# Performance work log

Measured on AMD Instinct MI355X. Metric: run time of the kernel, lower is better.

Reference implementation:

```python
import jax, jax.numpy as jnp
import numpy as np

N, D, R, E = 20000, 256, 12, 200000  # nodes, feat dim, relation labels, edges


def setup_inputs() -> dict:
    key = jax.random.key(0)
    ks = jax.random.split(key, 8)
    x = jax.random.normal(ks[0], (N, D), dtype=jnp.float32)
    dep_idx = jax.random.randint(ks[1], (E,), 0, N)
    rel_idx = jax.random.randint(ks[2], (E,), 0, R)
    gov_idx = jax.random.randint(ks[3], (E,), 0, N)
    # nn.Linear params: W is [out,in], y = x @ W.T + b
    W_self = jax.random.normal(ks[4], (D, D), dtype=jnp.float32) * 0.02
    b_self = jnp.zeros((D,), dtype=jnp.float32)
    # 2R relation weights: [0..R) forward labels, [R..2R) reversed '_r' labels
    W_rel = jax.random.normal(ks[5], (2 * R, D, D), dtype=jnp.float32) * 0.02
    b_rel = jax.random.normal(ks[6], (2 * R, D), dtype=jnp.float32) * 0.02
    return {"x": x, "dep_idx": dep_idx, "rel_idx": rel_idx, "gov_idx": gov_idx,
            "W_self": W_self, "b_self": b_self, "W_rel": W_rel, "b_rel": b_rel}


def reference(x, dep_idx, rel_idx, gov_idx, W_self, b_self, W_rel, b_rel):
    R_ = W_rel.shape[0] // 2
    # self transform for every node
    out = x @ W_self.T + b_self  # [N, D]
    # all-relation transform, grouped GEMM instead of per-edge Linear calls
    T = jnp.einsum('nd,rod->nro', x, W_rel)  # [N, 2R, D]
    # forward edges: dependent += W[rel] @ x[governor] + b[rel]
    msg_f = T[gov_idx, rel_idx] + b_rel[rel_idx]          # [E, D]
    # reverse edges: governor += W[rel_r] @ x[dependent] + b[rel_r]
    msg_r = T[dep_idx, rel_idx + R_] + b_rel[rel_idx + R_]  # [E, D]
    out = out.at[dep_idx].add(msg_f).at[gov_idx].add(msg_r)
    return jax.nn.relu(out)
```

## Files before the change

kernel.cpp:

```cpp
#include <hip/hip_runtime.h>
#include <cstdint>
#include <cstddef>

#define DD 256
#define NSLOT 25
#define SELFSLOT 12

typedef unsigned short u16;
typedef __bf16 bf16t;
typedef bf16t bf16x8 __attribute__((ext_vector_type(8)));
typedef unsigned short us8 __attribute__((ext_vector_type(8)));
typedef unsigned short us4 __attribute__((ext_vector_type(4)));
typedef float f32x4 __attribute__((ext_vector_type(4)));

__device__ __forceinline__ u16 f2bf(float f) {
    uint32_t u = __builtin_bit_cast(uint32_t, f);
    u += 0x7FFFu + ((u >> 16) & 1u);
    return (u16)(u >> 16);
}
__device__ __forceinline__ float bf2f(u16 h) {
    uint32_t u = ((uint32_t)h) << 16;
    return __builtin_bit_cast(float, u);
}

__global__ void k_prep(const float* __restrict__ x, const float* __restrict__ W_rel,
                       const float* __restrict__ W_self, const float* __restrict__ b_self,
                       const float* __restrict__ b_rel,
                       u16* __restrict__ xb, u16* __restrict__ Wb, float* __restrict__ ba,
                       const int* __restrict__ dep, const int* __restrict__ rel,
                       const int* __restrict__ gov, int E, int N, int SG,
                       int* __restrict__ flag, int* __restrict__ bcnt, int NDD) {
    if (blockIdx.x < 1024) {
        const int s0 = NDD;
        const int s1 = s0 + 12 * 65536;
        const int s2 = s1 + 65536;
        const int s3 = s2 + 12 * 65536;
        const int s4 = s3 + NSLOT * DD;
        int i = blockIdx.x * 256 + threadIdx.x;
        int st = 1024 * 256;
        for (; i < s4; i += st) {
            if (i < s0) {
                xb[i] = f2bf(x[i]);
            } else if (i < s1) {
                int k = i - s0; Wb[k] = f2bf(W_rel[k]);
            } else if (i < s2) {
                int k = i - s1; Wb[12 * 65536 + k] = f2bf(W_self[k]);
            } else if (i < s3) {
                int k = i - s2; Wb[13 * 65536 + k] = f2bf(W_rel[12 * 65536 + k]);
            } else {
                int k = i - s3;
                float v;
                if (k < 12 * DD) v = b_rel[k];
                else if (k < 13 * DD) v = b_self[k - 12 * DD];
                else v = b_rel[k - DD];
                ba[k] = v;
            }
        }
    } else {
        int i = (blockIdx.x - 1024) * 256 + threadIdx.x;
        int st = 512 * 256;
        for (int j = i; j < E; j += st) {
            int r = rel[j], d = dep[j], g = gov[j];
            flag[r * N + g] = 1;
            flag[(13 + r) * N + d] = 1;
            atomicAdd(&bcnt[(r / SG) * N + d], 1);
            atomicAdd(&bcnt[((13 + r) / SG) * N + g], 1);
        }
        for (int j = i; j < N; j += st) flag[SELFSLOT * N + j] = 1;
    }
}

__global__ void k_scan1d(const int* __restrict__ A, int* __restrict__ outA,
                         int* __restrict__ bsumA, int lenA, int nbA,
                         const int* __restrict__ B, int* __restrict__ outB,
                         int* __restrict__ bsumB, int lenB) {
    __shared__ int sm[256];
    const int* in; int* outp; int* bs; int len; int lb;
    if ((int)blockIdx.x < nbA) { in = A; outp = outA; bs = bsumA; len = lenA; lb = blockIdx.x; }
    else { in = B; outp = outB; bs = bsumB; len = lenB; lb = blockIdx.x - nbA; }
    int tid = threadIdx.x;
    int i = lb * 256 + tid;
    int v = (i < len) ? in[i] : 0;
    sm[tid] = v;
    __syncthreads();
    for (int off = 1; off < 256; off <<= 1) {
        int t = (tid >= off) ? sm[tid - off] : 0;
        __syncthreads();
        sm[tid] += t;
        __syncthreads();
    }
    if (i < len) outp[i] = sm[tid] - v;
    if (tid == 255) bs[lb] = sm[255];
}

__global__ void k_scan2d(const int* __restrict__ bsumA, int* __restrict__ bbasA, int nbA,
                         const int* __restrict__ bsumB, int* __restrict__ bbasB, int nbB) {
    __shared__ int sm[256];
    int t = threadIdx.x;
    for (int which = 0; which < 2; ++which) {
        const int* bsum = which ? bsumB : bsumA;
        int* bbase = which ? bbasB : bbasA;
        int nb = which ? nbB : nbA;
        int pre[8];
        int tot = 0;
        for (int j = 0; j < 8; ++j) {
            int idx = t * 8 + j;
            int v = (idx < nb) ? bsum[idx] : 0;
            pre[j] = tot;
            tot += v;
        }
        sm[t] = tot;
        __syncthreads();
        for (int off = 1; off < 256; off <<= 1) {
            int x = (t >= off) ? sm[t - off] : 0;
            __syncthreads();
            sm[t] += x;
            __syncthreads();
        }
        int base = sm[t] - tot;
        for (int j = 0; j < 8; ++j) {
            int idx = t * 8 + j;
            if (idx < nb) bbase[idx] = base + pre[j];
        }
        __syncthreads();
    }
}

__global__ void k_scan3d(int* __restrict__ pos, const int* __restrict__ bbasA,
                         const int* __restrict__ flag, int NN, int N,
                         int* __restrict__ rksrc,
                         int* __restrict__ bcsr, int* __restrict__ bcur,
                         const int* __restrict__ bbasB, int B2, int E2) {
    int i = blockIdx.x * 256 + threadIdx.x;
    if (i < NN) {
        int v = pos[i] + bbasA[i >> 8];
        pos[i] = v;
        if (i == NN - 1) pos[NN] = v + flag[i];
        if (flag[i]) {
            int slot = i / N;
            rksrc[v] = i - slot * N;
        }
    }
    if (i < B2) {
        int v = bcsr[i] + bbasB[i >> 8];
        bcsr[i] = v;
        bcur[i] = v;
    }
    if (i == 0) bcsr[B2] = E2;
}

__global__ void k_scatter(const int* __restrict__ dep, const int* __restrict__ rel,
                          const int* __restrict__ gov, int E, int N, int SG,
                          const int* __restrict__ pos,
                          int* __restrict__ cursor, int* __restrict__ epay) {
    int i = blockIdx.x * blockDim.x + threadIdx.x;
    int st = gridDim.x * blockDim.x;
    for (; i < E; i += st) {
        int r = rel[i], d = dep[i], g = gov[i];
        int g0 = r / SG;
        int p = atomicAdd(&cursor[g0 * N + d], 1);
        epay[p] = pos[r * N + g] - pos[g0 * SG * N];
        int gs = 13 + r;
        int g1 = gs / SG;
        int q = atomicAdd(&cursor[g1 * N + g], 1);
        epay[q] = pos[gs * N + d] - pos[g1 * SG * N];
    }
}

__global__ __launch_bounds__(256, 4) void k_T(
    const u16* __restrict__ xb, const u16* __restrict__ Wb, const float* __restrict__ ba,
    const int* __restrict__ pos, const int* __restrict__ rksrc, u16* __restrict__ T,
    int N, int gslot0, int Sg) {
    __shared__ u16 sm[2 * 128 * 72];
    __shared__ int s_src[128];
    u16 (*As)[72] = (u16(*)[72])sm;
    u16 (*Bs)[72] = (u16(*)[72])(sm + 128 * 72);

    const int bx = blockIdx.x;
    const int mtile = bx / (2 * Sg);
    const int rem = bx - mtile * 2 * Sg;
    const int slot = rem >> 1;
    const int n0 = (rem & 1) * 128;
    const int gslot = gslot0 + slot;
    const int u0 = pos[gslot * N];
    const int used = pos[(gslot + 1) * N] - u0;
    const int row0 = mtile * 128;
    if (row0 >= used) return;
    const int gbase = pos[gslot0 * N];
    const int tid = threadIdx.x;

    if (tid < 128) {
        int r = row0 + tid;
        s_src[tid] = rksrc[u0 + ((r < used) ? r : (used - 1))];
    }
    __syncthreads();

    const int lane = tid & 63, wv = tid >> 6;
    const int wr = wv & 1, wc = wv >> 1;
    const int l15 = lane & 15, quad = lane >> 4;
    const int srow = tid >> 1, sh = (tid & 1) * 32;
    const u16* bgp = Wb + ((size_t)gslot << 16) + (size_t)(n0 + srow) * DD + sh;

    f32x4 acc[4][4] = {};
    for (int kb = 0; kb < DD; kb += 64) {
        {
            const us8* ga = (const us8*)(xb + (size_t)s_src[srow] * DD + kb + sh);
            us8 a0 = ga[0], a1 = ga[1], a2 = ga[2], a3 = ga[3];
            *(us8*)&As[srow][sh]      = a0;
            *(us8*)&As[srow][sh + 8]  = a1;
            *(us8*)&As[srow][sh + 16] = a2;
            *(us8*)&As[srow][sh + 24] = a3;
            const us8* gb = (const us8*)(bgp + kb);
            us8 b0 = gb[0], b1 = gb[1], b2 = gb[2], b3 = gb[3];
            *(us8*)&Bs[srow][sh]      = b0;
            *(us8*)&Bs[srow][sh + 8]  = b1;
            *(us8*)&Bs[srow][sh + 16] = b2;
            *(us8*)&Bs[srow][sh + 24] = b3;
        }
        __syncthreads();
        #pragma unroll
        for (int ks = 0; ks < 2; ++ks) {
            const int kk = ks * 32 + quad * 8;
            bf16x8 af[4], bfv[4];
            #pragma unroll
            for (int mt = 0; mt < 4; ++mt)
                af[mt] = __builtin_bit_cast(bf16x8, *(const us8*)&As[wr * 64 + mt * 16 + l15][kk]);
            #pragma unroll
            for (int nt = 0; nt < 4; ++nt)
                bfv[nt] = __builtin_bit_cast(bf16x8, *(const us8*)&Bs[wc * 64 + nt * 16 + l15][kk]);
            #pragma unroll
            for (int nt = 0; nt < 4; ++nt)
                #pragma unroll
                for (int mt = 0; mt < 4; ++mt)
                    acc[nt][mt] = __builtin_amdgcn_mfma_f32_16x16x32_bf16(
                        bfv[nt], af[mt], acc[nt][mt], 0, 0, 0);
        }
        __syncthreads();
    }

    f32x4 bb[4];
    #pragma unroll
    for (int nt = 0; nt < 4; ++nt)
        bb[nt] = *(const f32x4*)(ba + gslot * DD + n0 + wc * 64 + nt * 16 + quad * 4);
    u16* trb = sm + wv * (64 * 72);
    #pragma unroll
    for (int mt = 0; mt < 4; ++mt)
        #pragma unroll
        for (int nt = 0; nt < 4; ++nt) {
            us4 t4;
            #pragma unroll
            for (int j = 0; j < 4; ++j) t4[j] = f2bf(acc[nt][mt][j] + bb[nt][j]);
            *(us4*)&trb[(size_t)(mt * 16 + l15) * 72 + nt * 16 + quad * 4] = t4;
        }
    __syncthreads();
    const int trow0 = u0 - gbase + row0 + wr * 64;
    const int half = lane & 1;
    #pragma unroll
    for (int it = 0; it < 2; ++it) {
        int r = it * 32 + (lane >> 1);
        if (row0 + wr * 64 + r < used) {
            const us8* sp = (const us8*)(trb + r * 72 + half * 32);
            us8 v0 = sp[0], v1 = sp[1], v2 = sp[2], v3 = sp[3];
            us8* dp = (us8*)(T + (size_t)(trow0 + r) * DD + n0 + wc * 64 + half * 32);
            dp[0] = v0; dp[1] = v1; dp[2] = v2; dp[3] = v3;
        }
    }
}

__global__ __launch_bounds__(256) void k_gather(
    const u16* __restrict__ T, const int* __restrict__ epay,
    const int* __restrict__ csr, const int* __restrict__ pos,
    float* __restrict__ out, int N, int bktBase, int selfKeyBase, int gfN,
    int first, int last) {
    int wid = (blockIdx.x * 256 + threadIdx.x) >> 6;
    if (wid >= N) return;
    int feat = (threadIdx.x & 63) * 4;
    f32x4 a = {0.0f, 0.0f, 0.0f, 0.0f};
    if (!first) a = *(const f32x4*)(out + (size_t)wid * DD + feat);
    if (selfKeyBase >= 0) {
        int p = pos[selfKeyBase + wid] - pos[gfN];
        us4 v = *(const us4*)(T + (size_t)p * DD + feat);
        a[0] += bf2f(v[0]); a[1] += bf2f(v[1]); a[2] += bf2f(v[2]); a[3] += bf2f(v[3]);
    }
    int beg = csr[bktBase + wid], end = csr[bktBase + wid + 1];
    f32x4 b = {0, 0, 0, 0}, c = {0, 0, 0, 0}, d4 = {0, 0, 0, 0};
    int j = beg;
    for (; j + 3 < end; j += 4) {
        int p0 = epay[j], p1 = epay[j + 1], p2 = epay[j + 2], p3 = epay[j + 3];
        us4 v0 = *(const us4*)(T + (size_t)p0 * DD + feat);
        us4 v1 = *(const us4*)(T + (size_t)p1 * DD + feat);
        us4 v2 = *(const us4*)(T + (size_t)p2 * DD + feat);
        us4 v3 = *(const us4*)(T + (size_t)p3 * DD + feat);
        a[0] += bf2f(v0[0]); a[1] += bf2f(v0[1]); a[2] += bf2f(v0[2]); a[3] += bf2f(v0[3]);
        b[0] += bf2f(v1[0]); b[1] += bf2f(v1[1]); b[2] += bf2f(v1[2]); b[3] += bf2f(v1[3]);
        c[0] += bf2f(v2[0]); c[1] += bf2f(v2[1]); c[2] += bf2f(v2[2]); c[3] += bf2f(v2[3]);
        d4[0] += bf2f(v3[0]); d4[1] += bf2f(v3[1]); d4[2] += bf2f(v3[2]); d4[3] += bf2f(v3[3]);
    }
    for (; j < end; ++j) {
        int p0 = epay[j];
        us4 v0 = *(const us4*)(T + (size_t)p0 * DD + feat);
        a[0] += bf2f(v0[0]); a[1] += bf2f(v0[1]); a[2] += bf2f(v0[2]); a[3] += bf2f(v0[3]);
    }
    a[0] += b[0] + c[0] + d4[0];
    a[1] += b[1] + c[1] + d4[1];
    a[2] += b[2] + c[2] + d4[2];
    a[3] += b[3] + c[3] + d4[3];
    if (last) {
        a[0] = fmaxf(a[0], 0.0f); a[1] = fmaxf(a[1], 0.0f);
        a[2] = fmaxf(a[2], 0.0f); a[3] = fmaxf(a[3], 0.0f);
    }
    *(f32x4*)(out + (size_t)wid * DD + feat) = a;
}

extern "C" void kernel_launch(void* const* d_in, const int* in_sizes, int n_in,
                              void* d_out, int out_size, void* d_ws, size_t ws_size,
                              hipStream_t stream) {
    const float* x      = (const float*)d_in[0];
    const int*   dep    = (const int*)  d_in[1];
    const int*   rel    = (const int*)  d_in[2];
    const int*   gov    = (const int*)  d_in[3];
    const float* W_self = (const float*)d_in[4];
    const float* b_self = (const float*)d_in[5];
    const float* W_rel  = (const float*)d_in[6];
    const float* b_rel  = (const float*)d_in[7];
    float* out = (float*)d_out;

    const int N  = in_sizes[0] / DD;
    const int E  = in_sizes[1];
    const int NN = NSLOT * N;

    char* w = (char*)d_ws;
    auto alloc = [&](size_t bytes) {
        char* p = w;
        w += (bytes + 255) & ~(size_t)255;
        return p;
    };
    u16* xb    = (u16*)alloc((size_t)N * DD * sizeof(u16));
    u16* Wb    = (u16*)alloc((size_t)NSLOT * DD * DD * sizeof(u16));
    float* ba  = (float*)alloc((size_t)NSLOT * DD * sizeof(float));
    int* flag  = (int*)alloc((size_t)NN * sizeof(int));
    int* pos   = (int*)alloc(((size_t)NN + 1) * sizeof(int));
    int* rksrc = (int*)alloc(((size_t)2 * E + N) * sizeof(int));
    int* bcnt  = (int*)alloc((size_t)6 * N * sizeof(int));
    int* bcsr  = (int*)alloc(((size_t)6 * N + 1) * sizeof(int));
    int* bcur  = (int*)alloc((size_t)6 * N * sizeof(int));
    int* bsumA = (int*)alloc((size_t)2048 * sizeof(int));
    int* bbasA = (int*)alloc((size_t)2048 * sizeof(int));
    int* bsumB = (int*)alloc((size_t)2048 * sizeof(int));
    int* bbasB = (int*)alloc((size_t)2048 * sizeof(int));
    int* epay  = (int*)alloc((size_t)2 * E * sizeof(int));

    size_t used = (size_t)(w - (char*)d_ws);
    size_t avail = (ws_size > used) ? (ws_size - used) : 0;

    int NGROUP = 2, SG = 13;
    for (int ng = 1; ng <= 5; ++ng) {
        int sg = (NSLOT + ng - 1) / ng;
        size_t maxB = 0;
        for (int g = 0; g < ng; ++g) {
            int s0 = g * sg, s1 = s0 + sg; if (s1 > NSLOT) s1 = NSLOT;
            if (s0 >= NSLOT) break;
            int hasSelf = (s0 <= SELFSLOT && SELFSLOT < s1) ? 1 : 0;
            size_t rels = (size_t)(s1 - s0 - hasSelf);
            size_t rows = rels * N; if (rows > (size_t)2 * E) rows = (size_t)2 * E;
            rows += hasSelf ? (size_t)N : 0;
            if (rows > maxB) maxB = rows;
        }
        if (maxB * ((size_t)DD * 2) <= avail) { NGROUP = ng; SG = sg; break; }
        NGROUP = ng + 1; SG = (NSLOT + NGROUP - 1) / NGROUP;
    }
    u16* T = (u16*)w;
    const int B2 = NGROUP * N;

    hipMemsetAsync(flag, 0, (size_t)NN * sizeof(int), stream);
    hipMemsetAsync(bcnt, 0, (size_t)B2 * sizeof(int), stream);
    k_prep<<<1536, 256, 0, stream>>>(x, W_rel, W_self, b_self, b_rel, xb, Wb, ba,
                                     dep, rel, gov, E, N, SG, flag, bcnt, N * DD);

    const int nbA = (NN + 255) / 256;
    const int nbB = (B2 + 255) / 256;
    k_scan1d<<<nbA + nbB, 256, 0, stream>>>(flag, pos, bsumA, NN, nbA, bcnt, bcsr, bsumB, B2);
    k_scan2d<<<1, 256, 0, stream>>>(bsumA, bbasA, nbA, bsumB, bbasB, nbB);
    k_scan3d<<<nbA, 256, 0, stream>>>(pos, bbasA, flag, NN, N, rksrc, bcsr, bcur, bbasB, B2, 2 * E);

    k_scatter<<<(E + 255) / 256, 256, 0, stream>>>(dep, rel, gov, E, N, SG, pos, bcur, epay);

    const int tilesPerSlot = (N + 127) / 128;
    const int gBlocks = (N + 3) / 4;
    for (int g = 0; g < NGROUP; ++g) {
        int s0 = g * SG;
        if (s0 >= NSLOT) break;
        int Sg = NSLOT - s0; if (Sg > SG) Sg = SG;
        k_T<<<dim3(tilesPerSlot * Sg * 2), 256, 0, stream>>>(
            xb, Wb, ba, pos, rksrc, T, N, s0, Sg);
        int hasSelf = (s0 <= SELFSLOT && SELFSLOT < s0 + Sg);
        k_gather<<<gBlocks, 256, 0, stream>>>(
            T, epay, bcsr, pos, out, N, g * N,
            hasSelf ? SELFSLOT * N : -1, s0 * N,
            (g == 0) ? 1 : 0, (g == NGROUP - 1) ? 1 : 0);
    }
}
```

Before: 269.6 us.

## Fuse edge scatter into first GEMM launch and unroll gather loop by eight

Removes the standalone k_scatter launch and runs edge bucketing in 256 extra blocks at the front of the first k_T grid, so the scatter overlaps the relation-transform GEMM. The gather loop is also unrolled from four to eight edges per iteration, with a two-edge tail, to keep more loads in flight. This saves one launch and lets atomics overlap with compute, at the cost of extra registers in the gather kernel and scatter blocks competing with GEMM blocks for CUs.

```diff
diff --git a/kernel.cpp b/kernel.cpp
--- a/kernel.cpp
+++ b/kernel.cpp
@@ -149,34 +149,35 @@
     if (i == 0) bcsr[B2] = E2;
 }
 
-__global__ void k_scatter(const int* __restrict__ dep, const int* __restrict__ rel,
-                          const int* __restrict__ gov, int E, int N, int SG,
-                          const int* __restrict__ pos,
-                          int* __restrict__ cursor, int* __restrict__ epay) {
-    int i = blockIdx.x * blockDim.x + threadIdx.x;
-    int st = gridDim.x * blockDim.x;
-    for (; i < E; i += st) {
-        int r = rel[i], d = dep[i], g = gov[i];
-        int g0 = r / SG;
-        int p = atomicAdd(&cursor[g0 * N + d], 1);
-        epay[p] = pos[r * N + g] - pos[g0 * SG * N];
-        int gs = 13 + r;
-        int g1 = gs / SG;
-        int q = atomicAdd(&cursor[g1 * N + g], 1);
-        epay[q] = pos[gs * N + d] - pos[g1 * SG * N];
-    }
-}
-
 __global__ __launch_bounds__(256, 4) void k_T(
     const u16* __restrict__ xb, const u16* __restrict__ Wb, const float* __restrict__ ba,
     const int* __restrict__ pos, const int* __restrict__ rksrc, u16* __restrict__ T,
-    int N, int gslot0, int Sg) {
+    int N, int gslot0, int Sg,
+    const int* __restrict__ dep, const int* __restrict__ rel, const int* __restrict__ gov,
+    int E, int SG, int* __restrict__ bcur, int* __restrict__ epay, int nScat) {
     __shared__ u16 sm[2 * 128 * 72];
     __shared__ int s_src[128];
     u16 (*As)[72] = (u16(*)[72])sm;
     u16 (*Bs)[72] = (u16(*)[72])(sm + 128 * 72);
 
-    const int bx = blockIdx.x;
+    const int tid = threadIdx.x;
+    if ((int)blockIdx.x < nScat) {
+        int i = blockIdx.x * 256 + tid;
+        int st = nScat * 256;
+        for (; i < E; i += st) {
+            int r = rel[i], d = dep[i], g = gov[i];
+            int g0 = r / SG;
+            int p = atomicAdd(&bcur[g0 * N + d], 1);
+            epay[p] = pos[r * N + g] - pos[g0 * SG * N];
+            int gs = 13 + r;
+            int g1 = gs / SG;
+            int q = atomicAdd(&bcur[g1 * N + g], 1);
+            epay[q] = pos[gs * N + d] - pos[g1 * SG * N];
+        }
+        return;
+    }
+
+    const int bx = blockIdx.x - nScat;
     const int mtile = bx / (2 * Sg);
     const int rem = bx - mtile * 2 * Sg;
     const int slot = rem >> 1;
@@ -187,7 +188,6 @@
     const int row0 = mtile * 128;
     if (row0 >= used) return;
     const int gbase = pos[gslot0 * N];
-    const int tid = threadIdx.x;
 
     if (tid < 128) {
         int r = row0 + tid;
@@ -285,29 +285,43 @@
     int beg = csr[bktBase + wid], end = csr[bktBase + wid + 1];
     f32x4 b = {0, 0, 0, 0}, c = {0, 0, 0, 0}, d4 = {0, 0, 0, 0};
     int j = beg;
-    for (; j + 3 < end; j += 4) {
-        int p0 = epay[j], p1 = epay[j + 1], p2 = epay[j + 2], p3 = epay[j + 3];
+    for (; j + 7 < end; j += 8) {
+        int p0 = epay[j],     p1 = epay[j + 1], p2 = epay[j + 2], p3 = epay[j + 3];
+        int p4 = epay[j + 4], p5 = epay[j + 5], p6 = epay[j + 6], p7 = epay[j + 7];
         us4 v0 = *(const us4*)(T + (size_t)p0 * DD + feat);
         us4 v1 = *(const us4*)(T + (size_t)p1 * DD + feat);
         us4 v2 = *(const us4*)(T + (size_t)p2 * DD + feat);
         us4 v3 = *(const us4*)(T + (size_t)p3 * DD + feat);
-        a[0] += bf2f(v0[0]); a[1] += bf2f(v0[1]); a[2] += bf2f(v0[2]); a[3] += bf2f(v0[3]);
-        b[0] += bf2f(v1[0]); b[1] += bf2f(v1[1]); b[2] += bf2f(v1[2]); b[3] += bf2f(v1[3]);
-        c[0] += bf2f(v2[0]); c[1] += bf2f(v2[1]); c[2] += bf2f(v2[2]); c[3] += bf2f(v2[3]);
-        d4[0] += bf2f(v3[0]); d4[1] += bf2f(v3[1]); d4[2] += bf2f(v3[2]); d4[3] += bf2f(v3[3]);
-    }
-    for (; j < end; ++j) {
+        us4 v4 = *(const us4*)(T + (size_t)p4 * DD + feat);
+        us4 v5 = *(const us4*)(T + (size_t)p5 * DD + feat);
+        us4 v6 = *(const us4*)(T + (size_t)p6 * DD + feat);
+        us4 v7 = *(const us4*)(T + (size_t)p7 * DD + feat);
+        #pragma unroll
+        for (int t = 0; t < 4; ++t) {
+            a[t]  += bf2f(v0[t]) + bf2f(v4[t]);
+            b[t]  += bf2f(v1[t]) + bf2f(v5[t]);
+            c[t]  += bf2f(v2[t]) + bf2f(v6[t]);
+            d4[t] += bf2f(v3[t]) + bf2f(v7[t]);
+        }
+    }
+    for (; j + 1 < end; j += 2) {
+        int p0 = epay[j], p1 = epay[j + 1];
+        us4 v0 = *(const us4*)(T + (size_t)p0 * DD + feat);
+        us4 v1 = *(const us4*)(T + (size_t)p1 * DD + feat);
+        #pragma unroll
+        for (int t = 0; t < 4; ++t) { a[t] += bf2f(v0[t]); b[t] += bf2f(v1[t]); }
+    }
+    if (j < end) {
         int p0 = epay[j];
         us4 v0 = *(const us4*)(T + (size_t)p0 * DD + feat);
-        a[0] += bf2f(v0[0]); a[1] += bf2f(v0[1]); a[2] += bf2f(v0[2]); a[3] += bf2f(v0[3]);
-    }
-    a[0] += b[0] + c[0] + d4[0];
-    a[1] += b[1] + c[1] + d4[1];
-    a[2] += b[2] + c[2] + d4[2];
-    a[3] += b[3] + c[3] + d4[3];
+        #pragma unroll
+        for (int t = 0; t < 4; ++t) a[t] += bf2f(v0[t]);
+    }
+    #pragma unroll
+    for (int t = 0; t < 4; ++t) a[t] += b[t] + c[t] + d4[t];
     if (last) {
-        a[0] = fmaxf(a[0], 0.0f); a[1] = fmaxf(a[1], 0.0f);
-        a[2] = fmaxf(a[2], 0.0f); a[3] = fmaxf(a[3], 0.0f);
+        #pragma unroll
+        for (int t = 0; t < 4; ++t) a[t] = fmaxf(a[t], 0.0f);
     }
     *(f32x4*)(out + (size_t)wid * DD + feat) = a;
 }
@@ -383,16 +397,16 @@
     k_scan2d<<<1, 256, 0, stream>>>(bsumA, bbasA, nbA, bsumB, bbasB, nbB);
     k_scan3d<<<nbA, 256, 0, stream>>>(pos, bbasA, flag, NN, N, rksrc, bcsr, bcur, bbasB, B2, 2 * E);
 
-    k_scatter<<<(E + 255) / 256, 256, 0, stream>>>(dep, rel, gov, E, N, SG, pos, bcur, epay);
-
     const int tilesPerSlot = (N + 127) / 128;
     const int gBlocks = (N + 3) / 4;
     for (int g = 0; g < NGROUP; ++g) {
         int s0 = g * SG;
         if (s0 >= NSLOT) break;
         int Sg = NSLOT - s0; if (Sg > SG) Sg = SG;
-        k_T<<<dim3(tilesPerSlot * Sg * 2), 256, 0, stream>>>(
-            xb, Wb, ba, pos, rksrc, T, N, s0, Sg);
+        int nScat = (g == 0) ? 256 : 0;
+        k_T<<<dim3(nScat + tilesPerSlot * Sg * 2), 256, 0, stream>>>(
+            xb, Wb, ba, pos, rksrc, T, N, s0, Sg,
+            dep, rel, gov, E, SG, bcur, epay, nScat);
         int hasSelf = (s0 <= SELFSLOT && SELFSLOT < s0 + Sg);
         k_gather<<<gBlocks, 256, 0, stream>>>(
             T, epay, bcsr, pos, out, N, g * N,
```

Result: faster. 260.7 us (median of 2 runs) (-3.3%).
